# Optimization experiments

Hardware: AMD Instinct MI355X
Metric: run time of the kernel (lower is better)

Reference implementation:

```python
import jax, jax.numpy as jnp
import numpy as np

EMPTY_IDX = 6  # relabeling of the original -1 ('EMPTY') expert to row 6 of the stacked tables


def setup_inputs() -> dict:
    key = jax.random.key(0)
    k1, k2, k3, k4, k5, k6 = jax.random.split(key, 6)
    B, L, H, T, E = 32, 2048, 768, 12, 7
    return {
        "sequence_output": jax.random.normal(k1, (B, L, H), dtype=jnp.float32),
        "module_net_w": jax.random.normal(k2, (E, H, H), dtype=jnp.float32),
        "span_net_w": jax.random.normal(k3, (E, H, 2), dtype=jnp.float32),
        "turns": jax.random.randint(k4, (B, T, 2), 0, L),
        "key_phrase_span": jax.random.randint(k5, (B, T, 2), 0, L),
        "module_index": jax.random.randint(k6, (B, T), 0, E),
    }


def reference(sequence_output, module_net_w, span_net_w, turns, key_phrase_span, module_index):
    seq = sequence_output            # [B, L, H]
    B, L, H = seq.shape
    T = turns.shape[1]
    f32 = seq.dtype

    eidx = module_index              # [B, T], 0..6 (6 == EMPTY, original -1)
    mod_mask = (eidx != EMPTY_IDX).astype(f32)            # module_index != -1
    start_pos = turns[:, :, 0]       # [B, T] turn start token positions
    turns_mask = (start_pos >= 0).astype(f32)             # turns[:,:,0] != -1

    # context_hidden_step = sequence_output[arange(B), start] for every step
    ctx = jnp.take_along_axis(seq, start_pos[:, :, None], axis=1)   # [B, T, H]

    # einsum('bh,bhz,blz->blz'): (ctx @ W_expert) broadcast-multiplied with seq.
    # Compute ctx @ W for ALL experts (tables are tiny), then gather per (b, t).
    cW_all = jnp.einsum('bth,ehz->btez', ctx, module_net_w)         # [B, T, 7, H]
    gidx = jnp.broadcast_to(eidx[:, :, None, None], (B, T, 1, H))
    cW = jnp.take_along_axis(cW_all, gidx, axis=2).squeeze(2)       # [B, T, H]

    span_w = span_net_w[eidx]        # [B, T, H, 2] per-sample expert span weights
    # logits[b,t,l,k] = sum_z seq[b,l,z] * cW[b,t,z] * span_w[b,t,z,k]
    v = cW[..., None] * span_w                                      # [B, T, H, 2]
    logits = jnp.einsum('blz,btzk->btlk', seq, v)                   # [B, T, L, 2]

    # CrossEntropyLoss(ignore_index=-1, reduction='none') over the L axis
    logsm = jax.nn.log_softmax(logits, axis=2)                      # [B, T, L, 2]
    tgt = key_phrase_span[:, :, :T][:, :T]  # [B, T, 2]
    tgt = key_phrase_span
    safe = jnp.clip(tgt, 0, L - 1)                                  # [B, T, 2]
    picked = jnp.take_along_axis(logsm, safe[:, :, None, :], axis=2).squeeze(2)  # [B, T, 2]
    ce = jnp.where(tgt >= 0, -picked, jnp.zeros((), f32))           # [B, T, 2]
    step_loss = 0.5 * (ce[..., 0] + ce[..., 1]) * mod_mask          # [B, T]

    loss = (step_loss * turns_mask).sum() / turns_mask.sum()
    return loss
```

## Files before the change

### kernel.cpp

```cpp
#include <hip/hip_runtime.h>
#include <math.h>

#define Bz 32
#define Lz 2048
#define Hz 768
#define Tz 12
#define Ez 7
#define EMPTYIDX 6
#define NCOL 24
#define LCHUNK 128
#define NCHUNK 16

__global__ void k0_compact(const int* __restrict__ midx,
                           int* __restrict__ off, int* __restrict__ items) {
    __shared__ int cnt[Ez];
    __shared__ int offs[Ez + 1];
    int tid = threadIdx.x;
    if (tid < Ez) cnt[tid] = 0;
    __syncthreads();
    int e = midx[tid];
    e = min(max(e, 0), Ez - 1);
    int r = atomicAdd(&cnt[e], 1);
    __syncthreads();
    if (tid == 0) {
        int acc = 0;
        for (int j = 0; j < Ez; ++j) { offs[j] = acc; acc += cnt[j]; }
        offs[Ez] = acc;
    }
    __syncthreads();
    items[offs[e] + r] = tid;
    if (tid <= Ez) off[tid] = offs[tid];
}

#define K1A_ZC 3
#define K1A_HB 48
#define K1A_HC 16
__global__ void k1a_cw(const float* __restrict__ seq, const float* __restrict__ W,
                       const int* __restrict__ turns,
                       const int* __restrict__ off, const int* __restrict__ items,
                       float* __restrict__ cW) {
    int bx = blockIdx.x;
    int e  = bx % Ez;
    int zc = (bx / Ez) % K1A_ZC;
    int hc = bx / (Ez * K1A_ZC);
    int z  = zc * 256 + threadIdx.x;
    int h0 = hc * K1A_HB;
    int off0 = off[e];
    int cnt  = off[e + 1] - off0;
    const float* Wb = W + ((size_t)e * Hz + h0) * Hz + z;
    float w[K1A_HB];
#pragma unroll
    for (int j = 0; j < K1A_HB; ++j) w[j] = Wb[(size_t)j * Hz];

    for (int n = 0; n < cnt; ++n) {
        int i  = items[off0 + n];
        int b  = i / Tz;
        int st = turns[2 * i];
        st = min(max(st, 0), Lz - 1);
        const float* c = seq + ((size_t)(b * Lz + st)) * Hz + h0;
        float acc = 0.f;
#pragma unroll
        for (int j = 0; j < K1A_HB; ++j) acc = fmaf(c[j], w[j], acc);
        atomicAdd(&cW[(size_t)i * Hz + z], acc);
    }
}

__global__ void k1b_v(const float* __restrict__ cW, const float* __restrict__ spanw,
                      const int* __restrict__ midx, float* __restrict__ v) {
    int idx = blockIdx.x * 256 + threadIdx.x;
    int i = idx / Hz;
    int z = idx - i * Hz;
    int e = midx[i];
    e = min(max(e, 0), Ez - 1);
    float cw = cW[idx];
    int b = i / Tz, t = i - b * Tz;
    size_t vb = ((size_t)(b * NCOL + t * 2)) * Hz + z;
    v[vb]      = cw * spanw[(e * Hz + z) * 2 + 0];
    v[vb + Hz] = cw * spanw[(e * Hz + z) * 2 + 1];
}

#define BK 64
#define ATS (BK + 4)
__global__ void k2_logits(const float* __restrict__ seq, const float* __restrict__ v,
                          float* __restrict__ pm, float* __restrict__ ps) {
    int bx = blockIdx.x;
    int b  = bx / NCHUNK;
    int ch = bx % NCHUNK;
    int l0 = ch * LCHUNK;
    int tid = threadIdx.x;
    int rg = tid >> 3;
    int cg = tid & 7;
    __shared__ float at[LCHUNK][ATS];
    __shared__ float vt[NCOL][ATS];
    __shared__ float red_m[NCOL][33];
    __shared__ float red_s[NCOL][33];
    float acc[4][3];
#pragma unroll
    for (int r = 0; r < 4; ++r)
#pragma unroll
        for (int j = 0; j < 3; ++j) acc[r][j] = 0.f;

    const float* A = seq + ((size_t)b * Lz + l0) * Hz;
    const float* V = v + (size_t)b * NCOL * Hz;

    for (int k0 = 0; k0 < Hz; k0 += BK) {
#pragma unroll
        for (int p = 0; p < 8; ++p) {
            int j  = tid + p * 256;
            int r  = j >> 4, c4 = j & 15;
            float4 x = *(const float4*)&A[(size_t)r * Hz + k0 + c4 * 4];
            *(float4*)&at[r][c4 * 4] = x;
        }
        {
            int j = tid;
            int c = j >> 4, q = j & 15;
            *(float4*)&vt[c][q * 4] = *(const float4*)&V[(size_t)c * Hz + k0 + q * 4];
            if (tid < 128) {
                j = tid + 256; c = j >> 4; q = j & 15;
                *(float4*)&vt[c][q * 4] = *(const float4*)&V[(size_t)c * Hz + k0 + q * 4];
            }
        }
        __syncthreads();
#pragma unroll
        for (int kk = 0; kk < BK; kk += 4) {
            float4 a0 = *(const float4*)&at[rg +  0][kk];
            float4 a1 = *(const float4*)&at[rg + 32][kk];
            float4 a2 = *(const float4*)&at[rg + 64][kk];
            float4 a3 = *(const float4*)&at[rg + 96][kk];
            float4 v0 = *(const float4*)&vt[cg * 3 + 0][kk];
            float4 v1 = *(const float4*)&vt[cg * 3 + 1][kk];
            float4 v2 = *(const float4*)&vt[cg * 3 + 2][kk];
#define DOT(ACC, AV, VV) ACC = fmaf(AV.w, VV.w, fmaf(AV.z, VV.z, fmaf(AV.y, VV.y, fmaf(AV.x, VV.x, ACC))))
            DOT(acc[0][0], a0, v0); DOT(acc[0][1], a0, v1); DOT(acc[0][2], a0, v2);
            DOT(acc[1][0], a1, v0); DOT(acc[1][1], a1, v1); DOT(acc[1][2], a1, v2);
            DOT(acc[2][0], a2, v0); DOT(acc[2][1], a2, v1); DOT(acc[2][2], a2, v2);
            DOT(acc[3][0], a3, v0); DOT(acc[3][1], a3, v1); DOT(acc[3][2], a3, v2);
#undef DOT
        }
        __syncthreads();
    }
#pragma unroll
    for (int j = 0; j < 3; ++j) {
        int c = cg * 3 + j;
        float m = fmaxf(fmaxf(acc[0][j], acc[1][j]), fmaxf(acc[2][j], acc[3][j]));
        float s = expf(acc[0][j] - m) + expf(acc[1][j] - m) +
                  expf(acc[2][j] - m) + expf(acc[3][j] - m);
        red_m[c][rg] = m;
        red_s[c][rg] = s;
    }
    __syncthreads();
    if (tid < NCOL) {
        int c = tid;
        float m = red_m[c][0];
        for (int r = 1; r < 32; ++r) m = fmaxf(m, red_m[c][r]);
        float s = 0.f;
        for (int r = 0; r < 32; ++r) s += red_s[c][r] * expf(red_m[c][r] - m);
        pm[((size_t)b * NCOL + c) * NCHUNK + ch] = m;
        ps[((size_t)b * NCOL + c) * NCHUNK + ch] = s;
    }
}

__global__ void k3_picked(const float* __restrict__ seq, const float* __restrict__ v,
                          const int* __restrict__ kps, float* __restrict__ picked) {
    int i = blockIdx.x;
    int b = i / Tz, t = i % Tz;
    int lane = threadIdx.x;
    for (int k = 0; k < 2; ++k) {
        int tgt  = kps[2 * i + k];
        int safe = min(max(tgt, 0), Lz - 1);
        const float* srow = seq + ((size_t)b * Lz + safe) * Hz;
        const float* vcol = v + ((size_t)(b * NCOL + t * 2 + k)) * Hz;
        float sum = 0.f;
#pragma unroll
        for (int q = 0; q < Hz / 64; ++q) {
            int z = lane + q * 64;
            sum = fmaf(srow[z], vcol[z], sum);
        }
        for (int o = 32; o > 0; o >>= 1) sum += __shfl_down(sum, o, 64);
        if (lane == 0) picked[b * NCOL + t * 2 + k] = sum;
    }
}

__global__ void k4_final(const int* __restrict__ midx, const int* __restrict__ turns,
                         const int* __restrict__ kps,
                         const float* __restrict__ pm, const float* __restrict__ ps,
                         const float* __restrict__ picked, float* __restrict__ out) {
    int tid = threadIdx.x;
    int i = tid;
    int b = i / Tz, t = i % Tz;
    int e = midx[i];
    float modm  = (e != EMPTYIDX) ? 1.f : 0.f;
    float tmask = (turns[2 * i] >= 0) ? 1.f : 0.f;
    float ce[2];
#pragma unroll
    for (int k = 0; k < 2; ++k) {
        int c = t * 2 + k;
        const float* pmr = pm + ((size_t)b * NCOL + c) * NCHUNK;
        const float* psr = ps + ((size_t)b * NCOL + c) * NCHUNK;
        float m = pmr[0];
        for (int chn = 1; chn < NCHUNK; ++chn) m = fmaxf(m, pmr[chn]);
        float s = 0.f;
        for (int chn = 0; chn < NCHUNK; ++chn) s += psr[chn] * expf(pmr[chn] - m);
        float lse = m + logf(s);
        int tgt = kps[2 * i + k];
        ce[k] = (tgt >= 0) ? (lse - picked[b * NCOL + c]) : 0.f;
    }
    float contrib = 0.5f * (ce[0] + ce[1]) * modm * tmask;

    __shared__ float wsum[6], wmask[6];
    float sl = contrib, sm = tmask;
    for (int o = 32; o > 0; o >>= 1) {
        sl += __shfl_down(sl, o, 64);
        sm += __shfl_down(sm, o, 64);
    }
    int w = tid >> 6, lane = tid & 63;
    if (lane == 0) { wsum[w] = sl; wmask[w] = sm; }
    __syncthreads();
    if (tid == 0) {
        float a = 0.f, mk = 0.f;
        for (int ww = 0; ww < 6; ++ww) { a += wsum[ww]; mk += wmask[ww]; }
        out[0] = a / mk;
    }
}

extern "C" void kernel_launch(void* const* d_in, const int* in_sizes, int n_in,
                              void* d_out, int out_size, void* d_ws, size_t ws_size,
                              hipStream_t stream) {
    const float* seq   = (const float*)d_in[0];
    const float* W     = (const float*)d_in[1];
    const float* spanw = (const float*)d_in[2];
    const int*   turns = (const int*)d_in[3];
    const int*   kps   = (const int*)d_in[4];
    const int*   midx  = (const int*)d_in[5];
    float* out = (float*)d_out;

    char* ws = (char*)d_ws;
    int*   off    = (int*)(ws + 0);
    int*   items  = (int*)(ws + 64);
    float* cW     = (float*)(ws + 2048);
    float* v      = (float*)(ws + 2048 + 1179648);
    float* pm     = (float*)(ws + 2048 + 1179648 + 2359296);
    float* ps     = (float*)(ws + 2048 + 1179648 + 2359296 + 49152);
    float* picked = (float*)(ws + 2048 + 1179648 + 2359296 + 98304);

    hipMemsetAsync(cW, 0, (size_t)384 * Hz * sizeof(float), stream);
    hipLaunchKernelGGL(k0_compact, dim3(1), dim3(Bz * Tz), 0, stream, midx, off, items);
    hipLaunchKernelGGL(k1a_cw, dim3(Ez * K1A_ZC * K1A_HC), dim3(256), 0, stream,
                       seq, W, turns, off, items, cW);
    hipLaunchKernelGGL(k1b_v, dim3((384 * Hz) / 256), dim3(256), 0, stream,
                       cW, spanw, midx, v);
    hipLaunchKernelGGL(k2_logits, dim3(Bz * NCHUNK), dim3(256), 0, stream, seq, v, pm, ps);
    hipLaunchKernelGGL(k3_picked, dim3(Bz * Tz), dim3(64), 0, stream, seq, v, kps, picked);
    hipLaunchKernelGGL(k4_final, dim3(1), dim3(Bz * Tz), 0, stream,
                       midx, turns, kps, pm, ps, picked, out);
}
```

Baseline: 370.7 us.

## Fuse expert compaction into cW kernel and register-prefetch logits GEMM tiles

Removes the separate single-block compaction kernel: each k1a block now scans module_index itself and builds its own list of matching items in shared memory, saving one launch and one dependency step. In k2_logits, the global loads for the next K-tile of seq and v are issued into registers right after the shared-memory stores, so they overlap with the FMA loop on the current tile. The trade-offs are redundant scanning of module_index in every k1a block and extra register pressure from the prefetched float4s, which may lower occupancy.

Result: slower. 428.6 us (+15.6%).

```diff
diff --git a/kernel.cpp b/kernel.cpp
--- a/kernel.cpp
+++ b/kernel.cpp
@@ -11,33 +11,11 @@
 #define LCHUNK 128
 #define NCHUNK 16
 
-__global__ void k0_compact(const int* __restrict__ midx,
-                           int* __restrict__ off, int* __restrict__ items) {
-    __shared__ int cnt[Ez];
-    __shared__ int offs[Ez + 1];
-    int tid = threadIdx.x;
-    if (tid < Ez) cnt[tid] = 0;
-    __syncthreads();
-    int e = midx[tid];
-    e = min(max(e, 0), Ez - 1);
-    int r = atomicAdd(&cnt[e], 1);
-    __syncthreads();
-    if (tid == 0) {
-        int acc = 0;
-        for (int j = 0; j < Ez; ++j) { offs[j] = acc; acc += cnt[j]; }
-        offs[Ez] = acc;
-    }
-    __syncthreads();
-    items[offs[e] + r] = tid;
-    if (tid <= Ez) off[tid] = offs[tid];
-}
-
 #define K1A_ZC 3
 #define K1A_HB 48
 #define K1A_HC 16
 __global__ void k1a_cw(const float* __restrict__ seq, const float* __restrict__ W,
-                       const int* __restrict__ turns,
-                       const int* __restrict__ off, const int* __restrict__ items,
+                       const int* __restrict__ turns, const int* __restrict__ midx,
                        float* __restrict__ cW) {
     int bx = blockIdx.x;
     int e  = bx % Ez;
@@ -45,15 +23,30 @@
     int hc = bx / (Ez * K1A_ZC);
     int z  = zc * 256 + threadIdx.x;
     int h0 = hc * K1A_HB;
-    int off0 = off[e];
-    int cnt  = off[e + 1] - off0;
+    int tid = threadIdx.x;
+
+    __shared__ int itemsS[Bz * Tz];
+    __shared__ int cntS;
+    if (tid == 0) cntS = 0;
+    __syncthreads();
+    for (int i = tid; i < Bz * Tz; i += 256) {
+        int ei = midx[i];
+        ei = min(max(ei, 0), Ez - 1);
+        if (ei == e) {
+            int p = atomicAdd(&cntS, 1);
+            itemsS[p] = i;
+        }
+    }
+    __syncthreads();
+    int cnt = cntS;
+
     const float* Wb = W + ((size_t)e * Hz + h0) * Hz + z;
     float w[K1A_HB];
 #pragma unroll
     for (int j = 0; j < K1A_HB; ++j) w[j] = Wb[(size_t)j * Hz];
 
     for (int n = 0; n < cnt; ++n) {
-        int i  = items[off0 + n];
+        int i  = itemsS[n];
         int b  = i / Tz;
         int st = turns[2 * i];
         st = min(max(st, 0), Lz - 1);
@@ -103,24 +96,44 @@
     const float* A = seq + ((size_t)b * Lz + l0) * Hz;
     const float* V = v + (size_t)b * NCOL * Hz;
 
+    int ar = tid >> 4, ac4 = tid & 15;
+    float4 ra[8];
+    float4 rv0, rv1;
+#pragma unroll
+    for (int p = 0; p < 8; ++p) {
+        int j = tid + p * 256, r = j >> 4, c4 = j & 15;
+        ra[p] = *(const float4*)&A[(size_t)r * Hz + c4 * 4];
+    }
+    rv0 = *(const float4*)&V[(size_t)(tid >> 4) * Hz + (tid & 15) * 4];
+    if (tid < 128) {
+        int j = tid + 256;
+        rv1 = *(const float4*)&V[(size_t)(j >> 4) * Hz + (j & 15) * 4];
+    }
+
     for (int k0 = 0; k0 < Hz; k0 += BK) {
 #pragma unroll
         for (int p = 0; p < 8; ++p) {
-            int j  = tid + p * 256;
-            int r  = j >> 4, c4 = j & 15;
-            float4 x = *(const float4*)&A[(size_t)r * Hz + k0 + c4 * 4];
-            *(float4*)&at[r][c4 * 4] = x;
-        }
-        {
-            int j = tid;
-            int c = j >> 4, q = j & 15;
-            *(float4*)&vt[c][q * 4] = *(const float4*)&V[(size_t)c * Hz + k0 + q * 4];
+            int j = tid + p * 256, r = j >> 4, c4 = j & 15;
+            *(float4*)&at[r][c4 * 4] = ra[p];
+        }
+        *(float4*)&vt[tid >> 4][(tid & 15) * 4] = rv0;
+        if (tid < 128) {
+            int j = tid + 256;
+            *(float4*)&vt[j >> 4][(j & 15) * 4] = rv1;
+        }
+        __syncthreads();
+        if (k0 + BK < Hz) {
+#pragma unroll
+            for (int p = 0; p < 8; ++p) {
+                int j = tid + p * 256, r = j >> 4, c4 = j & 15;
+                ra[p] = *(const float4*)&A[(size_t)r * Hz + k0 + BK + c4 * 4];
+            }
+            rv0 = *(const float4*)&V[(size_t)(tid >> 4) * Hz + k0 + BK + (tid & 15) * 4];
             if (tid < 128) {
-                j = tid + 256; c = j >> 4; q = j & 15;
-                *(float4*)&vt[c][q * 4] = *(const float4*)&V[(size_t)c * Hz + k0 + q * 4];
+                int j = tid + 256;
+                rv1 = *(const float4*)&V[(size_t)(j >> 4) * Hz + k0 + BK + (j & 15) * 4];
             }
         }
-        __syncthreads();
 #pragma unroll
         for (int kk = 0; kk < BK; kk += 4) {
             float4 a0 = *(const float4*)&at[rg +  0][kk];
@@ -139,6 +152,7 @@
         }
         __syncthreads();
     }
+    (void)ar; (void)ac4;
 #pragma unroll
     for (int j = 0; j < 3; ++j) {
         int c = cg * 3 + j;
@@ -235,18 +249,15 @@
     float* out = (float*)d_out;
 
     char* ws = (char*)d_ws;
-    int*   off    = (int*)(ws + 0);
-    int*   items  = (int*)(ws + 64);
-    float* cW     = (float*)(ws + 2048);
-    float* v      = (float*)(ws + 2048 + 1179648);
-    float* pm     = (float*)(ws + 2048 + 1179648 + 2359296);
-    float* ps     = (float*)(ws + 2048 + 1179648 + 2359296 + 49152);
-    float* picked = (float*)(ws + 2048 + 1179648 + 2359296 + 98304);
+    float* cW     = (float*)(ws + 0);
+    float* v      = (float*)(ws + 1179648);
+    float* pm     = (float*)(ws + 1179648 + 2359296);
+    float* ps     = (float*)(ws + 1179648 + 2359296 + 49152);
+    float* picked = (float*)(ws + 1179648 + 2359296 + 98304);
 
     hipMemsetAsync(cW, 0, (size_t)384 * Hz * sizeof(float), stream);
-    hipLaunchKernelGGL(k0_compact, dim3(1), dim3(Bz * Tz), 0, stream, midx, off, items);
     hipLaunchKernelGGL(k1a_cw, dim3(Ez * K1A_ZC * K1A_HC), dim3(256), 0, stream,
-                       seq, W, turns, off, items, cW);
+                       seq, W, turns, midx, cW);
     hipLaunchKernelGGL(k1b_v, dim3((384 * Hz) / 256), dim3(256), 0, stream,
                        cW, spanw, midx, v);
     hipLaunchKernelGGL(k2_logits, dim3(Bz * NCHUNK), dim3(256), 0, stream, seq, v, pm, ps);
```
